# Kernel optimization log

Measured on AMD Instinct MI355X. Metric: run time of the kernel, lower is better.

Reference implementation:

```python
import jax, jax.numpy as jnp
import numpy as np

B, L_IMG, L_TXT = 2, 1024, 512
D_IMG, D_TXT = 2048, 1024
NH, NKV, HD = 16, 8, 128
MLP_IMG, MLP_TXT = 8192, 4096
SOFTCAP = 50.0
EPS = 1e-6

def rms_norm(x, scale):
    var = jnp.mean(jnp.square(x), axis=-1, keepdims=True)
    return x * jax.lax.rsqrt(var + EPS) * (1.0 + scale)

def rope(x, positions):
    # x: [B, L, N, H]; positions: [B, L]
    H = x.shape[-1]
    half = H // 2
    freq = jnp.exp(-jnp.log(10000.0) * (jnp.arange(half, dtype=jnp.float32) * 2.0 / H))
    theta = positions[:, :, None].astype(jnp.float32) * freq          # [B, L, half]
    sin = jnp.sin(theta)[:, :, None, :]
    cos = jnp.cos(theta)[:, :, None, :]
    x1, x2 = jnp.split(x, 2, axis=-1)
    return jnp.concatenate([x1 * cos - x2 * sin, x2 * cos + x1 * sin], axis=-1).astype(x.dtype)

def get_qkv(x_norm, positions, wq, wk, wv):
    b, l, _ = x_norm.shape
    q = (x_norm @ wq).reshape(b, l, NH, HD)
    k = (x_norm @ wk).reshape(b, l, NKV, HD)
    v = (x_norm @ wv).reshape(b, l, NKV, HD)
    q = rope(q, positions)
    k = rope(k, positions)
    q = q * (HD ** -0.5)  # query_pre_attn_norm = 'rsqrt_head_dim'
    return q, k, v

def joint_attention(q, k, v, mask):
    # q: [B,T,NH,HD]; k,v: [B,S,NKV,HD]; mask: [B,1,T,S] bool
    b, t, n, h = q.shape
    g = n // NKV
    qg = q.reshape(b, t, NKV, g, h)
    logits = jnp.einsum('btkgh,bskh->bkgts', qg, k)
    logits = jnp.tanh(logits / SOFTCAP) * SOFTCAP  # attn_logits_softcap
    logits = jnp.where(mask[:, :, None], logits, -1e30)  # [B,1,1,T,S] broadcast
    probs = jax.nn.softmax(logits, axis=-1)
    out = jnp.einsum('bkgts,bskh->btkgh', probs, v)
    return out.reshape(b, t, n, h)

def ffn(x, w_gate, w_up, w_down):
    return (jax.nn.gelu(x @ w_gate) * (x @ w_up)) @ w_down

def _mixture_post(attn_proj, residual, pre_ffw_scale, w_gate, w_up, w_down):
    # post_norms=False, dropout=0: h = mlp(norm(attn_proj + x)) + x
    h = attn_proj + residual
    h = rms_norm(h, pre_ffw_scale)
    h = ffn(h, w_gate, w_up, w_down)
    return h + residual

def _block(x_img, x_txt, attn_mask,
           img_pre_attn_scale, img_wq, img_wk, img_wv, img_wo,
           img_pre_ffw_scale, img_w_gate, img_w_up, img_w_down,
           txt_pre_attn_scale, txt_wq, txt_wk, txt_wv, txt_wo,
           txt_pre_ffw_scale, txt_w_gate, txt_w_up, txt_w_down):
    pos_img = jnp.arange(0, L_IMG, dtype=jnp.int32)[None, :]
    pos_txt = jnp.arange(L_IMG, L_IMG + L_TXT, dtype=jnp.int32)[None, :]
    qi, ki, vi = get_qkv(rms_norm(x_img, img_pre_attn_scale), pos_img, img_wq, img_wk, img_wv)
    qt, kt, vt = get_qkv(rms_norm(x_txt, txt_pre_attn_scale), pos_txt, txt_wq, txt_wk, txt_wv)
    q = jnp.concatenate([qi, qt], axis=1)
    k = jnp.concatenate([ki, kt], axis=1)
    v = jnp.concatenate([vi, vt], axis=1)
    attn = joint_attention(q, k, v, attn_mask)  # [B, T, NH, HD]
    b = attn.shape[0]
    attn_flat = attn.reshape(b, L_IMG + L_TXT, NH * HD)
    proj_img = attn_flat[:, :L_IMG, :] @ img_wo
    proj_txt = attn_flat[:, L_IMG:, :] @ txt_wo
    out_img = _mixture_post(proj_img, x_img, img_pre_ffw_scale, img_w_gate, img_w_up, img_w_down)
    out_txt = _mixture_post(proj_txt, x_txt, txt_pre_ffw_scale, txt_w_gate, txt_w_up, txt_w_down)
    return out_img, out_txt

def setup_inputs() -> dict:
    key = jax.random.key(0)
    ks = jax.random.split(key, 32)
    inner = NH * HD
    def w(k, shape, fan_in):
        return jax.random.normal(k, shape, dtype=jnp.float32) / np.sqrt(fan_in)
    inp = {
        'x_img': jax.random.normal(ks[0], (B, L_IMG, D_IMG), dtype=jnp.float32),
        'x_txt': jax.random.normal(ks[1], (B, L_TXT, D_TXT), dtype=jnp.float32),
        'attn_mask': jnp.ones((B, 1, L_IMG + L_TXT, L_IMG + L_TXT), dtype=bool),
        'img_pre_attn_scale': jnp.zeros((D_IMG,), jnp.float32),
        'img_wq': w(ks[2], (D_IMG, inner), D_IMG),
        'img_wk': w(ks[3], (D_IMG, NKV * HD), D_IMG),
        'img_wv': w(ks[4], (D_IMG, NKV * HD), D_IMG),
        'img_wo': w(ks[5], (inner, D_IMG), inner),
        'img_pre_ffw_scale': jnp.zeros((D_IMG,), jnp.float32),
        'img_w_gate': w(ks[6], (D_IMG, MLP_IMG), D_IMG),
        'img_w_up': w(ks[7], (D_IMG, MLP_IMG), D_IMG),
        'img_w_down': w(ks[8], (MLP_IMG, D_IMG), MLP_IMG),
        'txt_pre_attn_scale': jnp.zeros((D_TXT,), jnp.float32),
        'txt_wq': w(ks[9], (D_TXT, inner), D_TXT),
        'txt_wk': w(ks[10], (D_TXT, NKV * HD), D_TXT),
        'txt_wv': w(ks[11], (D_TXT, NKV * HD), D_TXT),
        'txt_wo': w(ks[12], (inner, D_TXT), inner),
        'txt_pre_ffw_scale': jnp.zeros((D_TXT,), jnp.float32),
        'txt_w_gate': w(ks[13], (D_TXT, MLP_TXT), D_TXT),
        'txt_w_up': w(ks[14], (D_TXT, MLP_TXT), D_TXT),
        'txt_w_down': w(ks[15], (MLP_TXT, D_TXT), MLP_TXT),
    }
    return inp

def reference(x_img, x_txt, attn_mask,
              img_pre_attn_scale, img_wq, img_wk, img_wv, img_wo,
              img_pre_ffw_scale, img_w_gate, img_w_up, img_w_down,
              txt_pre_attn_scale, txt_wq, txt_wk, txt_wv, txt_wo,
              txt_pre_ffw_scale, txt_w_gate, txt_w_up, txt_w_down):
    return _block(x_img, x_txt, attn_mask,
                  img_pre_attn_scale, img_wq, img_wk, img_wv, img_wo,
                  img_pre_ffw_scale, img_w_gate, img_w_up, img_w_down,
                  txt_pre_attn_scale, txt_wq, txt_wk, txt_wv, txt_wo,
                  txt_pre_ffw_scale, txt_w_gate, txt_w_up, txt_w_down)
```

## Files before the change

kernel.cpp:

```cpp
#include <hip/hip_runtime.h>
#include <hip/hip_bf16.h>


typedef __hip_bfloat16 bf16;
typedef __attribute__((ext_vector_type(8))) __bf16 bf16x8;
typedef __attribute__((ext_vector_type(4))) float f32x4;

#define DEV __device__ __forceinline__

static constexpr int TT = 1536;
static constexpr int NHQ = 16, NKVH = 8, HDM = 128;

DEV void async_load16(const void* g, void* l) {
  typedef const __attribute__((address_space(1))) void* gas_t;
  typedef __attribute__((address_space(3))) void* las_t;
  __builtin_amdgcn_global_load_lds((gas_t)g, (las_t)l, 16, 0, 0);
}

DEV f32x4 mfma16(bf16x8 a, bf16x8 b, f32x4 c) {
  return __builtin_amdgcn_mfma_f32_16x16x32_bf16(a, b, c, 0, 0, 0);
}

DEV float bf2f(bf16 x) { return __bfloat162float(x); }
DEV bf16  f2bf(float x) { return __float2bfloat16(x); }

struct TJob { const float* src; bf16* dst; int K; int N; };
struct TJobs { TJob j[14]; int cum[15]; };

__global__ __launch_bounds__(256) void wt_transpose(TJobs P) {
  __shared__ bf16 tile[64][65];
  int bid = blockIdx.x;
  int ji = 0;
  while (ji < 13 && bid >= P.cum[ji + 1]) ji++;
  const TJob jb = P.j[ji];
  int rel = bid - P.cum[ji];
  int ntc = jb.N >> 6;
  int tr = rel / ntc, tc = rel - tr * ntc;
  int r0 = tr << 6, c0 = tc << 6;
  int t = threadIdx.x;
  #pragma unroll
  for (int i = 0; i < 16; i++) {
    int idx = i * 256 + t;
    int r = idx >> 6, c = idx & 63;
    tile[c][r] = f2bf(jb.src[(size_t)(r0 + r) * jb.N + c0 + c]);
  }
  __syncthreads();
  #pragma unroll
  for (int i = 0; i < 16; i++) {
    int idx = i * 256 + t;
    int r = idx >> 6, c = idx & 63;
    jb.dst[(size_t)(c0 + r) * jb.K + r0 + c] = tile[r][c];
  }
}

__global__ __launch_bounds__(256) void transpose_v(const bf16* __restrict__ v_all,
                                                   bf16* __restrict__ vt) {
  int st = blockIdx.x, ht = blockIdx.y, bk = blockIdx.z;
  int b = bk >> 3, kv = bk & 7;
  __shared__ bf16 tile[64][65];
  int t = threadIdx.x;
  int s0 = st * 64, h0 = ht * 64;
  #pragma unroll
  for (int i = 0; i < 16; i++) {
    int idx = i * 256 + t;
    int r = idx >> 6, c = idx & 63;
    tile[c][r] = v_all[((size_t)(b * TT + s0 + r) * NKVH + kv) * HDM + h0 + c];
  }
  __syncthreads();
  #pragma unroll
  for (int i = 0; i < 16; i++) {
    int idx = i * 256 + t;
    int r = idx >> 6, c = idx & 63;
    vt[((size_t)bk * HDM + h0 + r) * TT + s0 + c] = tile[r][c];
  }
}

template <int DV>
__global__ __launch_bounds__(256) void rmsnorm_k(const float* __restrict__ x,
                                                 const float* __restrict__ sc,
                                                 bf16* __restrict__ out) {
  const int D = DV * 1024;
  int row = blockIdx.x, t = threadIdx.x;
  const float4* xr = reinterpret_cast<const float4*>(x + (size_t)row * D);
  float4 v[DV];
  float ss = 0.f;
  #pragma unroll
  for (int i = 0; i < DV; i++) {
    v[i] = xr[t + i * 256];
    ss += v[i].x * v[i].x + v[i].y * v[i].y + v[i].z * v[i].z + v[i].w * v[i].w;
  }
  #pragma unroll
  for (int o = 1; o < 64; o <<= 1) ss += __shfl_xor(ss, o);
  __shared__ float red[4];
  if ((t & 63) == 0) red[t >> 6] = ss;
  __syncthreads();
  float r = rsqrtf((red[0] + red[1] + red[2] + red[3]) * (1.0f / D) + 1e-6f);
  bf16* orow = out + (size_t)row * D;
  #pragma unroll
  for (int i = 0; i < DV; i++) {
    int c = (t + i * 256) * 4;
    orow[c + 0] = f2bf(v[i].x * r * (1.f + sc[c + 0]));
    orow[c + 1] = f2bf(v[i].y * r * (1.f + sc[c + 1]));
    orow[c + 2] = f2bf(v[i].z * r * (1.f + sc[c + 2]));
    orow[c + 3] = f2bf(v[i].w * r * (1.f + sc[c + 3]));
  }
}

template <int DV>
__global__ __launch_bounds__(256) void rmsnorm4_k(
    const float* __restrict__ p0, const float* __restrict__ p1,
    const float* __restrict__ p2, const float* __restrict__ p3,
    const float* __restrict__ x, const float* __restrict__ sc,
    bf16* __restrict__ out) {
  const int D = DV * 1024;
  int row = blockIdx.x, t = threadIdx.x;
  size_t rb = (size_t)row * (D / 4);
  const float4* r0 = reinterpret_cast<const float4*>(p0) + rb;
  const float4* r1 = reinterpret_cast<const float4*>(p1) + rb;
  const float4* r2 = reinterpret_cast<const float4*>(p2) + rb;
  const float4* r3 = reinterpret_cast<const float4*>(p3) + rb;
  const float4* xr = reinterpret_cast<const float4*>(x) + rb;
  float4 v[DV];
  float ss = 0.f;
  #pragma unroll
  for (int i = 0; i < DV; i++) {
    int idx = t + i * 256;
    float4 a = r0[idx], b = r1[idx], c = r2[idx], d = r3[idx], e = xr[idx];
    v[i] = make_float4(a.x + b.x + c.x + d.x + e.x, a.y + b.y + c.y + d.y + e.y,
                       a.z + b.z + c.z + d.z + e.z, a.w + b.w + c.w + d.w + e.w);
    ss += v[i].x * v[i].x + v[i].y * v[i].y + v[i].z * v[i].z + v[i].w * v[i].w;
  }
  #pragma unroll
  for (int o = 1; o < 64; o <<= 1) ss += __shfl_xor(ss, o);
  __shared__ float red[4];
  if ((t & 63) == 0) red[t >> 6] = ss;
  __syncthreads();
  float r = rsqrtf((red[0] + red[1] + red[2] + red[3]) * (1.0f / D) + 1e-6f);
  bf16* orow = out + (size_t)row * D;
  #pragma unroll
  for (int i = 0; i < DV; i++) {
    int c = (t + i * 256) * 4;
    orow[c + 0] = f2bf(v[i].x * r * (1.f + sc[c + 0]));
    orow[c + 1] = f2bf(v[i].y * r * (1.f + sc[c + 1]));
    orow[c + 2] = f2bf(v[i].z * r * (1.f + sc[c + 2]));
    orow[c + 3] = f2bf(v[i].w * r * (1.f + sc[c + 3]));
  }
}

__global__ __launch_bounds__(256) void rope_inplace(bf16* __restrict__ x, int lognh,
                                                    float scale) {
  int gid = blockIdx.x * 256 + threadIdx.x;
  int i = gid & 63;
  int rh = gid >> 6;
  int row = rh >> lognh;
  int pos = row >= TT ? row - TT : row;
  float fr = expf(-9.210340371976184f * ((float)(2 * i) * (1.0f / 128.0f)));
  float th = (float)pos * fr;
  float s, c;
  sincosf(th, &s, &c);
  bf16* p = x + (size_t)rh * HDM;
  float x1 = bf2f(p[i]), x2 = bf2f(p[i + 64]);
  p[i]      = f2bf((x1 * c - x2 * s) * scale);
  p[i + 64] = f2bf((x2 * c + x1 * s) * scale);
}

struct G8Job {
  const bf16* A; const bf16* B; bf16* Cb; float* Cf;
  int K, N, lda, ldb;
  int a_base, a_lsh, a_lskip;
  int c_base, c_lsh, c_lskip, c_stride;
};
struct G8Jobs { G8Job j[8]; int cum[9]; int nj; };

#define G8_BAR_MFMA(MH, NH)                                        \
  __builtin_amdgcn_s_barrier();                                    \
  asm volatile("s_waitcnt lgkmcnt(0)" ::: "memory");               \
  __builtin_amdgcn_sched_barrier(0);                               \
  __builtin_amdgcn_s_setprio(1);                                   \
  _Pragma("unroll")                                                \
  for (int i = 0; i < 4; i++)                                      \
    _Pragma("unroll")                                              \
    for (int nj2 = 0; nj2 < 2; nj2++)                              \
      _Pragma("unroll")                                            \
      for (int kk = 0; kk < 2; kk++)                               \
        acc[(MH)*4 + i][(NH)*2 + nj2] = mfma16(                    \
            afr[i][kk], bfr[(NH)*2 + nj2][kk],                     \
            acc[(MH)*4 + i][(NH)*2 + nj2]);                        \
  __builtin_amdgcn_s_setprio(0);                                   \
  __builtin_amdgcn_s_barrier();                                    \
  asm volatile("" ::: "memory");

__global__ __launch_bounds__(512, 2) void gemm8(G8Jobs P) {
  extern __shared__ __align__(16) bf16 lds8[];
  int bid = blockIdx.x;
  int ji = 0;
  while (ji < P.nj - 1 && bid >= P.cum[ji + 1]) ji++;
  const G8Job jb = P.j[ji];
  int rel = bid - P.cum[ji];
  int tn = jb.N >> 8;
  int bm = rel / tn, bn = rel - bm * tn;
  const int m0 = bm << 8, n0 = bn << 8;
  const int K = jb.K;
  const int nk = K >> 6;
// ... 59 lines not shown
    for (int ni = 0; ni < 2; ni++) {
      int rb = (browb + ni * 16 + lr) * 64;
      bfr[ni][0] = *reinterpret_cast<const bf16x8*>(bufB + rb + s0);
      bfr[ni][1] = *reinterpret_cast<const bf16x8*>(bufB + rb + s1);
    }
    G8_BAR_MFMA(0, 0)

    #pragma unroll
    for (int ni = 2; ni < 4; ni++) {
      int rb = (browb + ni * 16 + lr) * 64;
      bfr[ni][0] = *reinterpret_cast<const bf16x8*>(bufB + rb + s0);
      bfr[ni][1] = *reinterpret_cast<const bf16x8*>(bufB + rb + s1);
    }
    G8_BAR_MFMA(0, 1)

    #pragma unroll
    for (int i = 0; i < 4; i++) {
      int rb = ((i + 4) * 16 + lr) * 64;
      afr[i][0] = *reinterpret_cast<const bf16x8*>(bufA + rb + s0);
      afr[i][1] = *reinterpret_cast<const bf16x8*>(bufA + rb + s1);
    }
    if (st) { stage(t + 2, 2); stage(t + 2, 3); }
    G8_BAR_MFMA(1, 0)

    if (st) {
      stage(t + 2, 0); stage(t + 2, 1);
      asm volatile("s_waitcnt vmcnt(8)" ::: "memory");
    } else if (t == nk - 2) {
      asm volatile("s_waitcnt vmcnt(0)" ::: "memory");
    }
    G8_BAR_MFMA(1, 1)
  }

  if (jb.Cf) {
    #pragma unroll
    for (int mi = 0; mi < 8; mi++)
      #pragma unroll
      for (int jj = 0; jj < 4; jj++) {
        int m = m0 + wr * 128 + mi * 16 + lk * 4 + jj;
        float* drow = jb.Cf + (size_t)m * jb.c_stride + n0 + wc * 64;
        #pragma unroll
        for (int ni = 0; ni < 4; ni++) drow[ni * 16 + lr] = acc[mi][ni][jj];
      }
  } else {
    #pragma unroll
    for (int mi = 0; mi < 8; mi++)
      #pragma unroll
      for (int jj = 0; jj < 4; jj++) {
        int m = m0 + wr * 128 + mi * 16 + lk * 4 + jj;
        int crow = jb.c_base + m + ((m >> jb.c_lsh) * jb.c_lskip);
        bf16* drow = jb.Cb + (size_t)crow * jb.c_stride + n0 + wc * 64;
        #pragma unroll
        for (int ni = 0; ni < 4; ni++) drow[ni * 16 + lr] = f2bf(acc[mi][ni][jj]);
      }
  }
}

__global__ __launch_bounds__(256) void reduce_down(
    float* __restrict__ oi, const float* __restrict__ q1,
    const float* __restrict__ q2, const float* __restrict__ q3,
    const float* __restrict__ xi, int n4i,
    float* __restrict__ ot, const float* __restrict__ r1,
    const float* __restrict__ xt, int n4t) {
  int tot = n4i + n4t;
  for (int idx = blockIdx.x * 256 + threadIdx.x; idx < tot; idx += gridDim.x * 256) {
    if (idx < n4i) {
      float4 d = ((const float4*)oi)[idx];
      float4 a = ((const float4*)q1)[idx];
      float4 b = ((const float4*)q2)[idx];
      float4 c = ((const float4*)q3)[idx];
      float4 e = ((const float4*)xi)[idx];
      ((float4*)oi)[idx] = make_float4(d.x + a.x + b.x + c.x + e.x,
                                       d.y + a.y + b.y + c.y + e.y,
                                       d.z + a.z + b.z + c.z + e.z,
                                       d.w + a.w + b.w + c.w + e.w);
    } else {
      int i = idx - n4i;
      float4 d = ((const float4*)ot)[i];
      float4 a = ((const float4*)r1)[i];
      float4 e = ((const float4*)xt)[i];
      ((float4*)ot)[i] = make_float4(d.x + a.x + e.x, d.y + a.y + e.y,
                                     d.z + a.z + e.z, d.w + a.w + e.w);
    }
  }
}

__global__ __launch_bounds__(256) void gelu_mul(const bf16* __restrict__ gu_i,
                                                bf16* __restrict__ act_i,
                                                const bf16* __restrict__ gu_t,
                                                bf16* __restrict__ act_t) {
  const int IMG_CH = 2048 * 8192 / 8;
  const int TXT_CH = 1024 * 4096 / 8;
  int idx = blockIdx.x * 256 + threadIdx.x;
  int total = IMG_CH + TXT_CH;
  if (idx >= total) return;
  const bf16* base;
  bf16* abase;
  int half, ci;
  if (idx < IMG_CH) { base = gu_i; abase = act_i; half = 8192; ci = idx; }
  else              { base = gu_t; abase = act_t; half = 4096; ci = idx - IMG_CH; }
  int perrow = half / 8;
  int m = ci / perrow, n8 = ci - m * perrow;
  const bf16* gp = base + (size_t)m * (half * 2) + n8 * 8;
  const bf16* up = gp + half;
  bf16x8 g8 = *reinterpret_cast<const bf16x8*>(gp);
  bf16x8 u8 = *reinterpret_cast<const bf16x8*>(up);
  bf16x8 o8;
  #pragma unroll
  for (int i = 0; i < 8; i++) {
    float g = (float)g8[i], u = (float)u8[i];
    float t = tanhf(0.7978845608028654f * (g + 0.044715f * g * g * g));
    o8[i] = (__bf16)(0.5f * g * (1.f + t) * u);
  }
  *reinterpret_cast<bf16x8*>(abase + (size_t)m * half + n8 * 8) = o8;
}

__global__ __launch_bounds__(256) void attn_k(const bf16* __restrict__ q_all,
                                              const bf16* __restrict__ k_all,
                                              const bf16* __restrict__ vt,
                                              bf16* __restrict__ attn_o) {
  const int qt = blockIdx.x;
  const int n = blockIdx.y;
  const int b = blockIdx.z;
  const int kv = n >> 1;
  const int tid = threadIdx.x, w = tid >> 6, l = tid & 63;
  const int lr = l & 15, lk = l >> 4;
  __shared__ __align__(16) bf16 Ksm[64 * 128];
  __shared__ __align__(16) bf16 Vsm[128 * 64];
  __shared__ __align__(16) bf16 Psm[4][16][72];

  bf16x8 qf[4];
  {
    int t = qt * 64 + w * 16 + lr;
    const bf16* qp = q_all + ((size_t)(b * TT + t) * NHQ + n) * HDM;
    #pragma unroll
    for (int kk = 0; kk < 4; kk++)
      qf[kk] = *reinterpret_cast<const bf16x8*>(qp + kk * 32 + lk * 8);
  }
  f32x4 acc_o[8];
  #pragma unroll
  for (int i = 0; i < 8; i++) acc_o[i] = (f32x4){0.f, 0.f, 0.f, 0.f};
  float den[4] = {0.f, 0.f, 0.f, 0.f};

  for (int st = 0; st < TT / 64; st++) {
    __syncthreads();
    #pragma unroll
    for (int i = 0; i < 4; i++) {
// ... 77 lines not shown
  const float* sc_attn_t = (const float*)d_in[12];
  const float* wq_t = (const float*)d_in[13];
  const float* wk_t = (const float*)d_in[14];
  const float* wv_t = (const float*)d_in[15];
  const float* wo_t = (const float*)d_in[16];
  const float* sc_ffw_t = (const float*)d_in[17];
  const float* wg_t = (const float*)d_in[18];
  const float* wu_t = (const float*)d_in[19];
  const float* wd_t = (const float*)d_in[20];
  float* outp = (float*)d_out;
  float* outp_t = outp + (size_t)2 * 1024 * 2048;

  char* ws = (char*)d_ws;
  size_t off = 0;
  auto alloc = [&](size_t n) {
    char* p = ws + off;
    off += (n + 255) & ~(size_t)255;
    return p;
  };
  bf16* WqT_i = (bf16*)alloc((size_t)2048 * 2048 * 2);
  bf16* WkT_i = (bf16*)alloc((size_t)1024 * 2048 * 2);
  bf16* WvT_i = (bf16*)alloc((size_t)1024 * 2048 * 2);
  bf16* WoT_i = (bf16*)alloc((size_t)2048 * 2048 * 2);
  bf16* WguT_i = (bf16*)alloc((size_t)16384 * 2048 * 2);
  bf16* WdT_i = (bf16*)alloc((size_t)2048 * 8192 * 2);
  bf16* WqT_t = (bf16*)alloc((size_t)2048 * 1024 * 2);
  bf16* WkT_t = (bf16*)alloc((size_t)1024 * 1024 * 2);
  bf16* WvT_t = (bf16*)alloc((size_t)1024 * 1024 * 2);
  bf16* WoT_t = (bf16*)alloc((size_t)1024 * 2048 * 2);
  bf16* WguT_t = (bf16*)alloc((size_t)8192 * 1024 * 2);
  bf16* WdT_t = (bf16*)alloc((size_t)1024 * 4096 * 2);
  bf16* xn_i = (bf16*)alloc((size_t)2048 * 2048 * 2);
  bf16* xn_t = (bf16*)alloc((size_t)1024 * 1024 * 2);
  char* S = (char*)alloc((size_t)112 * 1024 * 1024);
  (void)ws_size;

  const size_t MB = 1024 * 1024;
  bf16* q_all = (bf16*)S;
  bf16* k_all = (bf16*)(S + 12 * MB);
  bf16* v_all = (bf16*)(S + 18 * MB);
  bf16* vtr   = (bf16*)(S + 24 * MB);
  bf16* attn_o= (bf16*)(S + 30 * MB);
  float* wp0 = (float*)(S + 42 * MB);
  float* wp1 = (float*)(S + 62 * MB);
  float* wp2 = (float*)(S + 82 * MB);
  float* wp3 = (float*)S;
  const size_t TXT_OFF = 16 * MB / 4;
  bf16* gu_i  = (bf16*)S;
  bf16* gu_t  = (bf16*)(S + 64 * MB);
  bf16* act_i = (bf16*)(S + 80 * MB);
  bf16* act_t = (bf16*)xn_i;
  float* dp1 = (float*)S;
  float* dp2 = (float*)(S + 16 * MB);
  float* dp3 = (float*)(S + 32 * MB);
  float* dpt = (float*)(S + 48 * MB);

  (void)hipFuncSetAttribute(reinterpret_cast<const void*>(gemm8),
                            hipFuncAttributeMaxDynamicSharedMemorySize, 131072);

  TJobs tj;
  auto setj = [&](int idx, const float* s, bf16* d, int K, int N) {
    tj.j[idx].src = s; tj.j[idx].dst = d; tj.j[idx].K = K; tj.j[idx].N = N;
  };
  setj(0, wq_i, WqT_i, 2048, 2048);
  setj(1, wk_i, WkT_i, 2048, 1024);
  setj(2, wv_i, WvT_i, 2048, 1024);
  setj(3, wo_i, WoT_i, 2048, 2048);
  setj(4, wg_i, WguT_i, 2048, 8192);
  setj(5, wu_i, WguT_i + (size_t)8192 * 2048, 2048, 8192);
  setj(6, wd_i, WdT_i, 8192, 2048);
  setj(7, wq_t, WqT_t, 1024, 2048);
  setj(8, wk_t, WkT_t, 1024, 1024);
  setj(9, wv_t, WvT_t, 1024, 1024);
  setj(10, wo_t, WoT_t, 2048, 1024);
  setj(11, wg_t, WguT_t, 1024, 4096);
  setj(12, wu_t, WguT_t + (size_t)4096 * 1024, 1024, 4096);
  setj(13, wd_t, WdT_t, 4096, 1024);
  tj.cum[0] = 0;
  for (int i = 0; i < 14; i++)
    tj.cum[i + 1] = tj.cum[i] + (tj.j[i].K >> 6) * (tj.j[i].N >> 6);
  wt_transpose<<<tj.cum[14], 256, 0, stream>>>(tj);

  rmsnorm_k<2><<<2048, 256, 0, stream>>>(x_img, sc_attn_i, xn_i);
  rmsnorm_k<1><<<1024, 256, 0, stream>>>(x_txt, sc_attn_t, xn_t);

  auto mk8b = [](const bf16* A, const bf16* B, bf16* Cb, int K, int N, int lda,
                 int ldb, int ab, int ash, int ask, int cb2, int csh, int csk,
                 int cstr) {
    G8Job g{};
    g.A = A; g.B = B; g.Cb = Cb; g.Cf = nullptr;
    g.K = K; g.N = N; g.lda = lda; g.ldb = ldb;
    g.a_base = ab; g.a_lsh = ash; g.a_lskip = ask;
    g.c_base = cb2; g.c_lsh = csh; g.c_lskip = csk; g.c_stride = cstr;
    return g;
  };
  auto mk8f = [](const bf16* A, const bf16* B, float* Cf, int K, int N, int lda,
                 int ldb, int ab, int ash, int ask, int cstr) {
    G8Job g{};
    g.A = A; g.B = B; g.Cb = nullptr; g.Cf = Cf;
    g.K = K; g.N = N; g.lda = lda; g.ldb = ldb;
    g.a_base = ab; g.a_lsh = ash; g.a_lskip = ask;
    g.c_base = 0; g.c_lsh = 30; g.c_lskip = 0; g.c_stride = cstr;
    return g;
  };
  auto launch8 = [&](G8Jobs& P, int nj, const int* Mt) {
    P.nj = nj;
    P.cum[0] = 0;
    for (int i = 0; i < nj; i++) P.cum[i + 1] = P.cum[i] + Mt[i] * (P.j[i].N >> 8);
    gemm8<<<P.cum[nj], 512, 131072, stream>>>(P);
  };

  {
    G8Jobs P;
    P.j[0] = mk8b(xn_i, WqT_i, q_all, 2048, 2048, 2048, 2048, 0, 30, 0, 0, 10, 512, 2048);
    P.j[1] = mk8b(xn_i, WkT_i, k_all, 2048, 1024, 2048, 2048, 0, 30, 0, 0, 10, 512, 1024);
    P.j[2] = mk8b(xn_i, WvT_i, v_all, 2048, 1024, 2048, 2048, 0, 30, 0, 0, 10, 512, 1024);
    P.j[3] = mk8b(xn_t, WqT_t, q_all, 1024, 2048, 1024, 1024, 0, 30, 0, 1024, 9, 1024, 2048);
    P.j[4] = mk8b(xn_t, WkT_t, k_all, 1024, 1024, 1024, 1024, 0, 30, 0, 1024, 9, 1024, 1024);
    P.j[5] = mk8b(xn_t, WvT_t, v_all, 1024, 1024, 1024, 1024, 0, 30, 0, 1024, 9, 1024, 1024);
    int Mt[6] = {8, 8, 8, 4, 4, 4};
    launch8(P, 6, Mt);
  }

  rope_inplace<<<12288, 256, 0, stream>>>(q_all, 4, 0.08838834764831845f);
  rope_inplace<<<6144, 256, 0, stream>>>(k_all, 3, 1.0f);

  transpose_v<<<dim3(24, 2, 16), 256, 0, stream>>>(v_all, vtr);

  attn_k<<<dim3(24, 16, 2), 256, 0, stream>>>(q_all, k_all, vtr, attn_o);

  {
    G8Jobs P;
    float* wp[4] = {wp0, wp1, wp2, wp3};
    for (int s = 0; s < 4; s++) {
      P.j[s] = mk8f(attn_o + s * 512, WoT_i + s * 512, wp[s], 512, 2048, 2048,
                    2048, 0, 10, 512, 2048);
      P.j[4 + s] = mk8f(attn_o + s * 512, WoT_t + s * 512, wp[s] + TXT_OFF, 512,
                        1024, 2048, 2048, 1024, 9, 1024, 1024);
    }
    int Mt[8] = {8, 8, 8, 8, 4, 4, 4, 4};
    launch8(P, 8, Mt);
  }

  rmsnorm4_k<2><<<2048, 256, 0, stream>>>(wp0, wp1, wp2, wp3, x_img, sc_ffw_i, xn_i);
  rmsnorm4_k<1><<<1024, 256, 0, stream>>>(wp0 + TXT_OFF, wp1 + TXT_OFF,
                                          wp2 + TXT_OFF, wp3 + TXT_OFF, x_txt,
                                          sc_ffw_t, xn_t);

  {
    G8Jobs P;
    P.j[0] = mk8b(xn_i, WguT_i, gu_i, 2048, 16384, 2048, 2048, 0, 30, 0, 0, 30, 0, 16384);
    int Mt[1] = {8};
    launch8(P, 1, Mt);
  }
  {
    G8Jobs P;
    P.j[0] = mk8b(xn_t, WguT_t, gu_t, 1024, 8192, 1024, 1024, 0, 30, 0, 0, 30, 0, 8192);
    int Mt[1] = {4};
    launch8(P, 1, Mt);
  }
  {
    int total = 2048 * 8192 / 8 + 1024 * 4096 / 8;
    gelu_mul<<<(total + 255) / 256, 256, 0, stream>>>(gu_i, act_i, gu_t, act_t);
  }

  {
    G8Jobs P;
    P.j[0] = mk8f(act_i,            WdT_i,            outp, 2048, 2048, 8192, 8192, 0, 30, 0, 2048);
    P.j[1] = mk8f(act_i + 2048,     WdT_i + 2048,     dp1,  2048, 2048, 8192, 8192, 0, 30, 0, 2048);
    P.j[2] = mk8f(act_i + 4096,     WdT_i + 4096,     dp2,  2048, 2048, 8192, 8192, 0, 30, 0, 2048);
    P.j[3] = mk8f(act_i + 6144,     WdT_i + 6144,     dp3,  2048, 2048, 8192, 8192, 0, 30, 0, 2048);
    P.j[4] = mk8f(act_t,            WdT_t,            outp_t, 2048, 1024, 4096, 4096, 0, 30, 0, 1024);
    P.j[5] = mk8f(act_t + 2048,     WdT_t + 2048,     dpt,  2048, 1024, 4096, 4096, 0, 30, 0, 1024);
    int Mt[6] = {8, 8, 8, 8, 4, 4};
    launch8(P, 6, Mt);
  }
  reduce_down<<<2048, 256, 0, stream>>>(outp, dp1, dp2, dp3, x_img, 2048 * 2048 / 4,
                                        outp_t, dpt, x_txt, 1024 * 1024 / 4);
}
```

Measured before the change: 688.4 us.

## Fuse GELU-gated multiply into gate/up GEMM epilogue and rebalance split-K

Gate and up weight rows are interleaved in 128-column blocks, so each gemm8 tile holds matching gate and up outputs. The epilogue swaps the up half through LDS and writes the GELU(g)*u bf16 activation directly, which removes the standalone gelu_mul kernel and the round trip of the wide gate/up intermediate through global memory. The output projection split-K drops from 4 to 2 partials, so the residual RMSNorm reads fewer buffers. The text down-projection goes from 2 to 4 split-K slices to add parallelism. The fused epilogue adds an LDS exchange and a barrier, and leaves half the waves idle during the writeback.

```diff
diff --git a/kernel.cpp b/kernel.cpp
--- a/kernel.cpp
+++ b/kernel.cpp
@@ -24,7 +24,7 @@
 DEV float bf2f(bf16 x) { return __bfloat162float(x); }
 DEV bf16  f2bf(float x) { return __float2bfloat16(x); }
 
-struct TJob { const float* src; bf16* dst; int K; int N; };
+struct TJob { const float* src; bf16* dst; int K; int N; int r_base, r_lsh, r_skip; };
 struct TJobs { TJob j[14]; int cum[15]; };
 
 __global__ __launch_bounds__(256) void wt_transpose(TJobs P) {
@@ -49,7 +49,9 @@
   for (int i = 0; i < 16; i++) {
     int idx = i * 256 + t;
     int r = idx >> 6, c = idx & 63;
-    jb.dst[(size_t)(c0 + r) * jb.K + r0 + c] = tile[r][c];
+    int n = c0 + r;
+    int phys = jb.r_base + n + ((n >> jb.r_lsh) * jb.r_skip);
+    jb.dst[(size_t)phys * jb.K + r0 + c] = tile[r][c];
   }
 }
 
@@ -107,9 +109,8 @@
 }
 
 template <int DV>
-__global__ __launch_bounds__(256) void rmsnorm4_k(
+__global__ __launch_bounds__(256) void rmsnorm2_k(
     const float* __restrict__ p0, const float* __restrict__ p1,
-    const float* __restrict__ p2, const float* __restrict__ p3,
     const float* __restrict__ x, const float* __restrict__ sc,
     bf16* __restrict__ out) {
   const int D = DV * 1024;
@@ -117,17 +118,15 @@
   size_t rb = (size_t)row * (D / 4);
   const float4* r0 = reinterpret_cast<const float4*>(p0) + rb;
   const float4* r1 = reinterpret_cast<const float4*>(p1) + rb;
-  const float4* r2 = reinterpret_cast<const float4*>(p2) + rb;
-  const float4* r3 = reinterpret_cast<const float4*>(p3) + rb;
   const float4* xr = reinterpret_cast<const float4*>(x) + rb;
   float4 v[DV];
   float ss = 0.f;
   #pragma unroll
   for (int i = 0; i < DV; i++) {
     int idx = t + i * 256;
-    float4 a = r0[idx], b = r1[idx], c = r2[idx], d = r3[idx], e = xr[idx];
-    v[i] = make_float4(a.x + b.x + c.x + d.x + e.x, a.y + b.y + c.y + d.y + e.y,
-                       a.z + b.z + c.z + d.z + e.z, a.w + b.w + c.w + d.w + e.w);
+    float4 a = r0[idx], b = r1[idx], e = xr[idx];
+    v[i] = make_float4(a.x + b.x + e.x, a.y + b.y + e.y,
+                       a.z + b.z + e.z, a.w + b.w + e.w);
     ss += v[i].x * v[i].x + v[i].y * v[i].y + v[i].z * v[i].z + v[i].w * v[i].w;
   }
   #pragma unroll
@@ -169,6 +168,7 @@
   int K, N, lda, ldb;
   int a_base, a_lsh, a_lskip;
   int c_base, c_lsh, c_lskip, c_stride;
+  int fuse;
 };
 struct G8Jobs { G8Job j[8]; int cum[9]; int nj; };
 
@@ -294,7 +294,41 @@
     G8_BAR_MFMA(1, 1)
   }
 
-  if (jb.Cf) {
+  if (jb.fuse) {
+    float* xch = reinterpret_cast<float*>(lds8);
+    if (wc >= 2) {
+      float* slot = xch + (wr * 2 + (wc - 2)) * 8192;
+      #pragma unroll
+      for (int mi = 0; mi < 8; mi++)
+        #pragma unroll
+        for (int jj = 0; jj < 4; jj++) {
+          int row = mi * 16 + lk * 4 + jj;
+          #pragma unroll
+          for (int ni = 0; ni < 4; ni++)
+            slot[row * 64 + ni * 16 + lr] = acc[mi][ni][jj];
+        }
+    }
+    __syncthreads();
+    if (wc < 2) {
+      const float* slot = xch + (wr * 2 + wc) * 8192;
+      int colbase = (n0 >> 1) + wc * 64;
+      #pragma unroll
+      for (int mi = 0; mi < 8; mi++)
+        #pragma unroll
+        for (int jj = 0; jj < 4; jj++) {
+          int m = m0 + wr * 128 + mi * 16 + lk * 4 + jj;
+          int row = mi * 16 + lk * 4 + jj;
+          bf16* drow = jb.Cb + (size_t)m * jb.c_stride + colbase;
+          #pragma unroll
+          for (int ni = 0; ni < 4; ni++) {
+            float g = acc[mi][ni][jj];
+            float u = slot[row * 64 + ni * 16 + lr];
+            float tt = tanhf(0.7978845608028654f * (g + 0.044715f * g * g * g));
+            drow[ni * 16 + lr] = f2bf(0.5f * g * (1.f + tt) * u);
+          }
+        }
+    }
+  } else if (jb.Cf) {
     #pragma unroll
     for (int mi = 0; mi < 8; mi++)
       #pragma unroll
@@ -319,18 +353,19 @@
 }
 
 __global__ __launch_bounds__(256) void reduce_down(
-    float* __restrict__ oi, const float* __restrict__ q1,
-    const float* __restrict__ q2, const float* __restrict__ q3,
+    float* __restrict__ oi, const float* __restrict__ a1,
+    const float* __restrict__ a2, const float* __restrict__ a3,
     const float* __restrict__ xi, int n4i,
-    float* __restrict__ ot, const float* __restrict__ r1,
+    float* __restrict__ ot, const float* __restrict__ b1,
+    const float* __restrict__ b2, const float* __restrict__ b3,
     const float* __restrict__ xt, int n4t) {
   int tot = n4i + n4t;
   for (int idx = blockIdx.x * 256 + threadIdx.x; idx < tot; idx += gridDim.x * 256) {
     if (idx < n4i) {
       float4 d = ((const float4*)oi)[idx];
-      float4 a = ((const float4*)q1)[idx];
-      float4 b = ((const float4*)q2)[idx];
-      float4 c = ((const float4*)q3)[idx];
+      float4 a = ((const float4*)a1)[idx];
+      float4 b = ((const float4*)a2)[idx];
+      float4 c = ((const float4*)a3)[idx];
       float4 e = ((const float4*)xi)[idx];
       ((float4*)oi)[idx] = make_float4(d.x + a.x + b.x + c.x + e.x,
                                        d.y + a.y + b.y + c.y + e.y,
@@ -339,42 +374,16 @@
     } else {
       int i = idx - n4i;
       float4 d = ((const float4*)ot)[i];
-      float4 a = ((const float4*)r1)[i];
+      float4 a = ((const float4*)b1)[i];
+      float4 b = ((const float4*)b2)[i];
+      float4 c = ((const float4*)b3)[i];
       float4 e = ((const float4*)xt)[i];
-      ((float4*)ot)[i] = make_float4(d.x + a.x + e.x, d.y + a.y + e.y,
-                                     d.z + a.z + e.z, d.w + a.w + e.w);
-    }
-  }
-}
-
-__global__ __launch_bounds__(256) void gelu_mul(const bf16* __restrict__ gu_i,
-                                                bf16* __restrict__ act_i,
-                                                const bf16* __restrict__ gu_t,
-                                                bf16* __restrict__ act_t) {
-  const int IMG_CH = 2048 * 8192 / 8;
-  const int TXT_CH = 1024 * 4096 / 8;
-  int idx = blockIdx.x * 256 + threadIdx.x;
-  int total = IMG_CH + TXT_CH;
-  if (idx >= total) return;
-  const bf16* base;
-  bf16* abase;
-  int half, ci;
-  if (idx < IMG_CH) { base = gu_i; abase = act_i; half = 8192; ci = idx; }
-  else              { base = gu_t; abase = act_t; half = 4096; ci = idx - IMG_CH; }
-  int perrow = half / 8;
-  int m = ci / perrow, n8 = ci - m * perrow;
-  const bf16* gp = base + (size_t)m * (half * 2) + n8 * 8;
-  const bf16* up = gp + half;
-  bf16x8 g8 = *reinterpret_cast<const bf16x8*>(gp);
-  bf16x8 u8 = *reinterpret_cast<const bf16x8*>(up);
-  bf16x8 o8;
-  #pragma unroll
-  for (int i = 0; i < 8; i++) {
-    float g = (float)g8[i], u = (float)u8[i];
-    float t = tanhf(0.7978845608028654f * (g + 0.044715f * g * g * g));
-    o8[i] = (__bf16)(0.5f * g * (1.f + t) * u);
-  }
-  *reinterpret_cast<bf16x8*>(abase + (size_t)m * half + n8 * 8) = o8;
+      ((float4*)ot)[i] = make_float4(d.x + a.x + b.x + c.x + e.x,
+                                     d.y + a.y + b.y + c.y + e.y,
+                                     d.z + a.z + b.z + c.z + e.z,
+                                     d.w + a.w + b.w + c.w + e.w);
+    }
+  }
 }
 
 __global__ __launch_bounds__(256) void attn_k(const bf16* __restrict__ q_all,
@@ -529,39 +538,39 @@
   bf16* attn_o= (bf16*)(S + 30 * MB);
   float* wp0 = (float*)(S + 42 * MB);
   float* wp1 = (float*)(S + 62 * MB);
-  float* wp2 = (float*)(S + 82 * MB);
-  float* wp3 = (float*)S;
   const size_t TXT_OFF = 16 * MB / 4;
-  bf16* gu_i  = (bf16*)S;
-  bf16* gu_t  = (bf16*)(S + 64 * MB);
-  bf16* act_i = (bf16*)(S + 80 * MB);
-  bf16* act_t = (bf16*)xn_i;
-  float* dp1 = (float*)S;
-  float* dp2 = (float*)(S + 16 * MB);
-  float* dp3 = (float*)(S + 32 * MB);
-  float* dpt = (float*)(S + 48 * MB);
+  bf16* act_i = (bf16*)S;
+  bf16* act_t = (bf16*)(S + 32 * MB);
+  float* dp1 = (float*)(S + 42 * MB);
+  float* dp2 = (float*)(S + 58 * MB);
+  float* dp3 = (float*)(S + 74 * MB);
+  float* dt1 = (float*)(S + 90 * MB);
+  float* dt2 = (float*)(S + 94 * MB);
+  float* dt3 = (float*)(S + 98 * MB);
 
   (void)hipFuncSetAttribute(reinterpret_cast<const void*>(gemm8),
                             hipFuncAttributeMaxDynamicSharedMemorySize, 131072);
 
   TJobs tj;
-  auto setj = [&](int idx, const float* s, bf16* d, int K, int N) {
+  auto setj = [&](int idx, const float* s, bf16* d, int K, int N, int rb, int rl,
+                  int rs) {
     tj.j[idx].src = s; tj.j[idx].dst = d; tj.j[idx].K = K; tj.j[idx].N = N;
+    tj.j[idx].r_base = rb; tj.j[idx].r_lsh = rl; tj.j[idx].r_skip = rs;
   };
-  setj(0, wq_i, WqT_i, 2048, 2048);
-  setj(1, wk_i, WkT_i, 2048, 1024);
-  setj(2, wv_i, WvT_i, 2048, 1024);
-  setj(3, wo_i, WoT_i, 2048, 2048);
-  setj(4, wg_i, WguT_i, 2048, 8192);
-  setj(5, wu_i, WguT_i + (size_t)8192 * 2048, 2048, 8192);
-  setj(6, wd_i, WdT_i, 8192, 2048);
-  setj(7, wq_t, WqT_t, 1024, 2048);
-  setj(8, wk_t, WkT_t, 1024, 1024);
-  setj(9, wv_t, WvT_t, 1024, 1024);
-  setj(10, wo_t, WoT_t, 2048, 1024);
-  setj(11, wg_t, WguT_t, 1024, 4096);
-  setj(12, wu_t, WguT_t + (size_t)4096 * 1024, 1024, 4096);
-  setj(13, wd_t, WdT_t, 4096, 1024);
+  setj(0, wq_i, WqT_i, 2048, 2048, 0, 30, 0);
+  setj(1, wk_i, WkT_i, 2048, 1024, 0, 30, 0);
+  setj(2, wv_i, WvT_i, 2048, 1024, 0, 30, 0);
+  setj(3, wo_i, WoT_i, 2048, 2048, 0, 30, 0);
+  setj(4, wg_i, WguT_i, 2048, 8192, 0, 7, 128);
+  setj(5, wu_i, WguT_i, 2048, 8192, 128, 7, 128);
+  setj(6, wd_i, WdT_i, 8192, 2048, 0, 30, 0);
+  setj(7, wq_t, WqT_t, 1024, 2048, 0, 30, 0);
+  setj(8, wk_t, WkT_t, 1024, 1024, 0, 30, 0);
+  setj(9, wv_t, WvT_t, 1024, 1024, 0, 30, 0);
+  setj(10, wo_t, WoT_t, 2048, 1024, 0, 30, 0);
+  setj(11, wg_t, WguT_t, 1024, 4096, 0, 7, 128);
+  setj(12, wu_t, WguT_t, 1024, 4096, 128, 7, 128);
+  setj(13, wd_t, WdT_t, 4096, 1024, 0, 30, 0);
   tj.cum[0] = 0;
   for (int i = 0; i < 14; i++)
     tj.cum[i + 1] = tj.cum[i] + (tj.j[i].K >> 6) * (tj.j[i].N >> 6);
@@ -572,12 +581,13 @@
 
   auto mk8b = [](const bf16* A, const bf16* B, bf16* Cb, int K, int N, int lda,
                  int ldb, int ab, int ash, int ask, int cb2, int csh, int csk,
-                 int cstr) {
+                 int cstr, int fuse) {
     G8Job g{};
     g.A = A; g.B = B; g.Cb = Cb; g.Cf = nullptr;
     g.K = K; g.N = N; g.lda = lda; g.ldb = ldb;
     g.a_base = ab; g.a_lsh = ash; g.a_lskip = ask;
     g.c_base = cb2; g.c_lsh = csh; g.c_lskip = csk; g.c_stride = cstr;
+    g.fuse = fuse;
     return g;
   };
   auto mk8f = [](const bf16* A, const bf16* B, float* Cf, int K, int N, int lda,
@@ -587,6 +597,7 @@
     g.K = K; g.N = N; g.lda = lda; g.ldb = ldb;
     g.a_base = ab; g.a_lsh = ash; g.a_lskip = ask;
     g.c_base = 0; g.c_lsh = 30; g.c_lskip = 0; g.c_stride = cstr;
+    g.fuse = 0;
     return g;
   };
   auto launch8 = [&](G8Jobs& P, int nj, const int* Mt) {
@@ -598,12 +609,12 @@
 
   {
     G8Jobs P;
-    P.j[0] = mk8b(xn_i, WqT_i, q_all, 2048, 2048, 2048, 2048, 0, 30, 0, 0, 10, 512, 2048);
-    P.j[1] = mk8b(xn_i, WkT_i, k_all, 2048, 1024, 2048, 2048, 0, 30, 0, 0, 10, 512, 1024);
-    P.j[2] = mk8b(xn_i, WvT_i, v_all, 2048, 1024, 2048, 2048, 0, 30, 0, 0, 10, 512, 1024);
-    P.j[3] = mk8b(xn_t, WqT_t, q_all, 1024, 2048, 1024, 1024, 0, 30, 0, 1024, 9, 1024, 2048);
-    P.j[4] = mk8b(xn_t, WkT_t, k_all, 1024, 1024, 1024, 1024, 0, 30, 0, 1024, 9, 1024, 1024);
-    P.j[5] = mk8b(xn_t, WvT_t, v_all, 1024, 1024, 1024, 1024, 0, 30, 0, 1024, 9, 1024, 1024);
+    P.j[0] = mk8b(xn_i, WqT_i, q_all, 2048, 2048, 2048, 2048, 0, 30, 0, 0, 10, 512, 2048, 0);
+    P.j[1] = mk8b(xn_i, WkT_i, k_all, 2048, 1024, 2048, 2048, 0, 30, 0, 0, 10, 512, 1024, 0);
+    P.j[2] = mk8b(xn_i, WvT_i, v_all, 2048, 1024, 2048, 2048, 0, 30, 0, 0, 10, 512, 1024, 0);
+    P.j[3] = mk8b(xn_t, WqT_t, q_all, 1024, 2048, 1024, 1024, 0, 30, 0, 1024, 9, 1024, 2048, 0);
+    P.j[4] = mk8b(xn_t, WkT_t, k_all, 1024, 1024, 1024, 1024, 0, 30, 0, 1024, 9, 1024, 1024, 0);
+    P.j[5] = mk8b(xn_t, WvT_t, v_all, 1024, 1024, 1024, 1024, 0, 30, 0, 1024, 9, 1024, 1024, 0);
     int Mt[6] = {8, 8, 8, 4, 4, 4};
     launch8(P, 6, Mt);
   }
@@ -617,50 +628,44 @@
 
   {
     G8Jobs P;
-    float* wp[4] = {wp0, wp1, wp2, wp3};
-    for (int s = 0; s < 4; s++) {
-      P.j[s] = mk8f(attn_o + s * 512, WoT_i + s * 512, wp[s], 512, 2048, 2048,
-                    2048, 0, 10, 512, 2048);
-      P.j[4 + s] = mk8f(attn_o + s * 512, WoT_t + s * 512, wp[s] + TXT_OFF, 512,
-                        1024, 2048, 2048, 1024, 9, 1024, 1024);
-    }
+    P.j[0] = mk8f(attn_o,        WoT_i,        wp0, 1024, 2048, 2048, 2048, 0, 10, 512, 2048);
+    P.j[1] = mk8f(attn_o + 1024, WoT_i + 1024, wp1, 1024, 2048, 2048, 2048, 0, 10, 512, 2048);
+    P.j[2] = mk8f(attn_o,        WoT_t,        wp0 + TXT_OFF, 1024, 1024, 2048, 2048, 1024, 9, 1024, 1024);
+    P.j[3] = mk8f(attn_o + 1024, WoT_t + 1024, wp1 + TXT_OFF, 1024, 1024, 2048, 2048, 1024, 9, 1024, 1024);
+    int Mt[4] = {8, 8, 4, 4};
+    launch8(P, 4, Mt);
+  }
+
+  rmsnorm2_k<2><<<2048, 256, 0, stream>>>(wp0, wp1, x_img, sc_ffw_i, xn_i);
+  rmsnorm2_k<1><<<1024, 256, 0, stream>>>(wp0 + TXT_OFF, wp1 + TXT_OFF, x_txt,
+                                          sc_ffw_t, xn_t);
+
+  {
+    G8Jobs P;
+    P.j[0] = mk8b(xn_i, WguT_i, act_i, 2048, 16384, 2048, 2048, 0, 30, 0, 0, 30, 0, 8192, 1);
+    int Mt[1] = {8};
+    launch8(P, 1, Mt);
+  }
+  {
+    G8Jobs P;
+    P.j[0] = mk8b(xn_t, WguT_t, act_t, 1024, 8192, 1024, 1024, 0, 30, 0, 0, 30, 0, 4096, 1);
+    int Mt[1] = {4};
+    launch8(P, 1, Mt);
+  }
+
+  {
+    G8Jobs P;
+    P.j[0] = mk8f(act_i,        WdT_i,        outp, 2048, 2048, 8192, 8192, 0, 30, 0, 2048);
+    P.j[1] = mk8f(act_i + 2048, WdT_i + 2048, dp1,  2048, 2048, 8192, 8192, 0, 30, 0, 2048);
+    P.j[2] = mk8f(act_i + 4096, WdT_i + 4096, dp2,  2048, 2048, 8192, 8192, 0, 30, 0, 2048);
+    P.j[3] = mk8f(act_i + 6144, WdT_i + 6144, dp3,  2048, 2048, 8192, 8192, 0, 30, 0, 2048);
+    P.j[4] = mk8f(act_t,        WdT_t,        outp_t, 1024, 1024, 4096, 4096, 0, 30, 0, 1024);
+    P.j[5] = mk8f(act_t + 1024, WdT_t + 1024, dt1,  1024, 1024, 4096, 4096, 0, 30, 0, 1024);
+    P.j[6] = mk8f(act_t + 2048, WdT_t + 2048, dt2,  1024, 1024, 4096, 4096, 0, 30, 0, 1024);
+    P.j[7] = mk8f(act_t + 3072, WdT_t + 3072, dt3,  1024, 1024, 4096, 4096, 0, 30, 0, 1024);
     int Mt[8] = {8, 8, 8, 8, 4, 4, 4, 4};
     launch8(P, 8, Mt);
   }
-
-  rmsnorm4_k<2><<<2048, 256, 0, stream>>>(wp0, wp1, wp2, wp3, x_img, sc_ffw_i, xn_i);
-  rmsnorm4_k<1><<<1024, 256, 0, stream>>>(wp0 + TXT_OFF, wp1 + TXT_OFF,
-                                          wp2 + TXT_OFF, wp3 + TXT_OFF, x_txt,
-                                          sc_ffw_t, xn_t);
-
-  {
-    G8Jobs P;
-    P.j[0] = mk8b(xn_i, WguT_i, gu_i, 2048, 16384, 2048, 2048, 0, 30, 0, 0, 30, 0, 16384);
-    int Mt[1] = {8};
-    launch8(P, 1, Mt);
-  }
-  {
-    G8Jobs P;
-    P.j[0] = mk8b(xn_t, WguT_t, gu_t, 1024, 8192, 1024, 1024, 0, 30, 0, 0, 30, 0, 8192);
-    int Mt[1] = {4};
-    launch8(P, 1, Mt);
-  }
-  {
-    int total = 2048 * 8192 / 8 + 1024 * 4096 / 8;
-    gelu_mul<<<(total + 255) / 256, 256, 0, stream>>>(gu_i, act_i, gu_t, act_t);
-  }
-
-  {
-    G8Jobs P;
-    P.j[0] = mk8f(act_i,            WdT_i,            outp, 2048, 2048, 8192, 8192, 0, 30, 0, 2048);
-    P.j[1] = mk8f(act_i + 2048,     WdT_i + 2048,     dp1,  2048, 2048, 8192, 8192, 0, 30, 0, 2048);
-    P.j[2] = mk8f(act_i + 4096,     WdT_i + 4096,     dp2,  2048, 2048, 8192, 8192, 0, 30, 0, 2048);
-    P.j[3] = mk8f(act_i + 6144,     WdT_i + 6144,     dp3,  2048, 2048, 8192, 8192, 0, 30, 0, 2048);
-    P.j[4] = mk8f(act_t,            WdT_t,            outp_t, 2048, 1024, 4096, 4096, 0, 30, 0, 1024);
-    P.j[5] = mk8f(act_t + 2048,     WdT_t + 2048,     dpt,  2048, 1024, 4096, 4096, 0, 30, 0, 1024);
-    int Mt[6] = {8, 8, 8, 8, 4, 4};
-    launch8(P, 6, Mt);
-  }
   reduce_down<<<2048, 256, 0, stream>>>(outp, dp1, dp2, dp3, x_img, 2048 * 2048 / 4,
-                                        outp_t, dpt, x_txt, 1024 * 1024 / 4);
-}
+                                        outp_t, dt1, dt2, dt3, x_txt, 1024 * 1024 / 4);
+}
```

Result: no change. 698.1 us (+1.4%).

## Rebalance split-K partitions and fuse img/txt gate-up GEMMs into one launch

Applied to the files above, without the earlier changes.

The output-projection split-K drops from four to two partitions, so the residual RMS norm reads two partial buffers instead of four. The image and text gate/up GEMMs now go out in a single grouped launch rather than two. GELU-mul writes its result in place into the gate half of the gate/up buffer, and the down projection reads it with stride 16384. The text down projection is split four ways instead of two, with its partial sums placed in transposed-weight buffers that are no longer needed. This trades fewer launches and less partial-sum traffic for longer per-tile K loops on the output projection, and it relies on reusing dead weight buffers as scratch.

```diff
diff --git a/kernel.cpp b/kernel.cpp
--- a/kernel.cpp
+++ b/kernel.cpp
@@ -107,9 +107,8 @@
 }
 
 template <int DV>
-__global__ __launch_bounds__(256) void rmsnorm4_k(
+__global__ __launch_bounds__(256) void rmsnorm2_k(
     const float* __restrict__ p0, const float* __restrict__ p1,
-    const float* __restrict__ p2, const float* __restrict__ p3,
     const float* __restrict__ x, const float* __restrict__ sc,
     bf16* __restrict__ out) {
   const int D = DV * 1024;
@@ -117,17 +116,15 @@
   size_t rb = (size_t)row * (D / 4);
   const float4* r0 = reinterpret_cast<const float4*>(p0) + rb;
   const float4* r1 = reinterpret_cast<const float4*>(p1) + rb;
-  const float4* r2 = reinterpret_cast<const float4*>(p2) + rb;
-  const float4* r3 = reinterpret_cast<const float4*>(p3) + rb;
   const float4* xr = reinterpret_cast<const float4*>(x) + rb;
   float4 v[DV];
   float ss = 0.f;
   #pragma unroll
   for (int i = 0; i < DV; i++) {
     int idx = t + i * 256;
-    float4 a = r0[idx], b = r1[idx], c = r2[idx], d = r3[idx], e = xr[idx];
-    v[i] = make_float4(a.x + b.x + c.x + d.x + e.x, a.y + b.y + c.y + d.y + e.y,
-                       a.z + b.z + c.z + d.z + e.z, a.w + b.w + c.w + d.w + e.w);
+    float4 a = r0[idx], b = r1[idx], e = xr[idx];
+    v[i] = make_float4(a.x + b.x + e.x, a.y + b.y + e.y,
+                       a.z + b.z + e.z, a.w + b.w + e.w);
     ss += v[i].x * v[i].x + v[i].y * v[i].y + v[i].z * v[i].z + v[i].w * v[i].w;
   }
   #pragma unroll
@@ -319,18 +316,19 @@
 }
 
 __global__ __launch_bounds__(256) void reduce_down(
-    float* __restrict__ oi, const float* __restrict__ q1,
-    const float* __restrict__ q2, const float* __restrict__ q3,
+    float* __restrict__ oi, const float* __restrict__ a1,
+    const float* __restrict__ a2, const float* __restrict__ a3,
     const float* __restrict__ xi, int n4i,
-    float* __restrict__ ot, const float* __restrict__ r1,
+    float* __restrict__ ot, const float* __restrict__ b1,
+    const float* __restrict__ b2, const float* __restrict__ b3,
     const float* __restrict__ xt, int n4t) {
   int tot = n4i + n4t;
   for (int idx = blockIdx.x * 256 + threadIdx.x; idx < tot; idx += gridDim.x * 256) {
     if (idx < n4i) {
       float4 d = ((const float4*)oi)[idx];
-      float4 a = ((const float4*)q1)[idx];
-      float4 b = ((const float4*)q2)[idx];
-      float4 c = ((const float4*)q3)[idx];
+      float4 a = ((const float4*)a1)[idx];
+      float4 b = ((const float4*)a2)[idx];
+      float4 c = ((const float4*)a3)[idx];
       float4 e = ((const float4*)xi)[idx];
       ((float4*)oi)[idx] = make_float4(d.x + a.x + b.x + c.x + e.x,
                                        d.y + a.y + b.y + c.y + e.y,
@@ -339,32 +337,34 @@
     } else {
       int i = idx - n4i;
       float4 d = ((const float4*)ot)[i];
-      float4 a = ((const float4*)r1)[i];
+      float4 a = ((const float4*)b1)[i];
+      float4 b = ((const float4*)b2)[i];
+      float4 c = ((const float4*)b3)[i];
       float4 e = ((const float4*)xt)[i];
-      ((float4*)ot)[i] = make_float4(d.x + a.x + e.x, d.y + a.y + e.y,
-                                     d.z + a.z + e.z, d.w + a.w + e.w);
-    }
-  }
-}
-
-__global__ __launch_bounds__(256) void gelu_mul(const bf16* __restrict__ gu_i,
-                                                bf16* __restrict__ act_i,
-                                                const bf16* __restrict__ gu_t,
-                                                bf16* __restrict__ act_t) {
+      ((float4*)ot)[i] = make_float4(d.x + a.x + b.x + c.x + e.x,
+                                     d.y + a.y + b.y + c.y + e.y,
+                                     d.z + a.z + b.z + c.z + e.z,
+                                     d.w + a.w + b.w + c.w + e.w);
+    }
+  }
+}
+
+__global__ __launch_bounds__(256) void gelu_mul(bf16* __restrict__ gu_i,
+                                                bf16* __restrict__ gu_t) {
   const int IMG_CH = 2048 * 8192 / 8;
   const int TXT_CH = 1024 * 4096 / 8;
   int idx = blockIdx.x * 256 + threadIdx.x;
   int total = IMG_CH + TXT_CH;
   if (idx >= total) return;
-  const bf16* base;
-  bf16* abase;
+  bf16* base;
   int half, ci;
-  if (idx < IMG_CH) { base = gu_i; abase = act_i; half = 8192; ci = idx; }
-  else              { base = gu_t; abase = act_t; half = 4096; ci = idx - IMG_CH; }
+  if (idx < IMG_CH) { base = gu_i; half = 8192; ci = idx; }
+  else              { base = gu_t; half = 4096; ci = idx - IMG_CH; }
+  int rowlen = half * 2;
   int perrow = half / 8;
   int m = ci / perrow, n8 = ci - m * perrow;
-  const bf16* gp = base + (size_t)m * (half * 2) + n8 * 8;
-  const bf16* up = gp + half;
+  bf16* gp = base + (size_t)m * rowlen + n8 * 8;
+  bf16* up = gp + half;
   bf16x8 g8 = *reinterpret_cast<const bf16x8*>(gp);
   bf16x8 u8 = *reinterpret_cast<const bf16x8*>(up);
   bf16x8 o8;
@@ -374,7 +374,7 @@
     float t = tanhf(0.7978845608028654f * (g + 0.044715f * g * g * g));
     o8[i] = (__bf16)(0.5f * g * (1.f + t) * u);
   }
-  *reinterpret_cast<bf16x8*>(abase + (size_t)m * half + n8 * 8) = o8;
+  *reinterpret_cast<bf16x8*>(gp) = o8;
 }
 
 __global__ __launch_bounds__(256) void attn_k(const bf16* __restrict__ q_all,
@@ -518,7 +518,9 @@
   bf16* WdT_t = (bf16*)alloc((size_t)1024 * 4096 * 2);
   bf16* xn_i = (bf16*)alloc((size_t)2048 * 2048 * 2);
   bf16* xn_t = (bf16*)alloc((size_t)1024 * 1024 * 2);
-  char* S = (char*)alloc((size_t)112 * 1024 * 1024);
+  float* h_i = (float*)alloc((size_t)2048 * 2048 * 4);
+  float* h_t = (float*)alloc((size_t)1024 * 1024 * 4);
+  char* S = (char*)alloc((size_t)84 * 1024 * 1024);
   (void)ws_size;
 
   const size_t MB = 1024 * 1024;
@@ -527,19 +529,16 @@
   bf16* v_all = (bf16*)(S + 18 * MB);
   bf16* vtr   = (bf16*)(S + 24 * MB);
   bf16* attn_o= (bf16*)(S + 30 * MB);
-  float* wp0 = (float*)(S + 42 * MB);
-  float* wp1 = (float*)(S + 62 * MB);
-  float* wp2 = (float*)(S + 82 * MB);
-  float* wp3 = (float*)S;
-  const size_t TXT_OFF = 16 * MB / 4;
+  float* wp1_i = (float*)S;
+  float* wp1_t = (float*)(S + 16 * MB);
   bf16* gu_i  = (bf16*)S;
   bf16* gu_t  = (bf16*)(S + 64 * MB);
-  bf16* act_i = (bf16*)(S + 80 * MB);
-  bf16* act_t = (bf16*)xn_i;
-  float* dp1 = (float*)S;
-  float* dp2 = (float*)(S + 16 * MB);
-  float* dp3 = (float*)(S + 32 * MB);
-  float* dpt = (float*)(S + 48 * MB);
+  float* dp1 = (float*)WguT_i;
+  float* dp2 = (float*)((char*)WguT_i + 16 * MB);
+  float* dp3 = (float*)((char*)WguT_i + 32 * MB);
+  float* dt1 = (float*)WguT_t;
+  float* dt2 = (float*)((char*)WguT_t + 4 * MB);
+  float* dt3 = (float*)((char*)WguT_t + 8 * MB);
 
   (void)hipFuncSetAttribute(reinterpret_cast<const void*>(gemm8),
                             hipFuncAttributeMaxDynamicSharedMemorySize, 131072);
@@ -617,50 +616,42 @@
 
   {
     G8Jobs P;
-    float* wp[4] = {wp0, wp1, wp2, wp3};
-    for (int s = 0; s < 4; s++) {
-      P.j[s] = mk8f(attn_o + s * 512, WoT_i + s * 512, wp[s], 512, 2048, 2048,
-                    2048, 0, 10, 512, 2048);
-      P.j[4 + s] = mk8f(attn_o + s * 512, WoT_t + s * 512, wp[s] + TXT_OFF, 512,
-                        1024, 2048, 2048, 1024, 9, 1024, 1024);
-    }
-    int Mt[8] = {8, 8, 8, 8, 4, 4, 4, 4};
-    launch8(P, 8, Mt);
-  }
-
-  rmsnorm4_k<2><<<2048, 256, 0, stream>>>(wp0, wp1, wp2, wp3, x_img, sc_ffw_i, xn_i);
-  rmsnorm4_k<1><<<1024, 256, 0, stream>>>(wp0 + TXT_OFF, wp1 + TXT_OFF,
-                                          wp2 + TXT_OFF, wp3 + TXT_OFF, x_txt,
-                                          sc_ffw_t, xn_t);
+    P.j[0] = mk8f(attn_o,        WoT_i,        h_i,   1024, 2048, 2048, 2048, 0, 10, 512, 2048);
+    P.j[1] = mk8f(attn_o + 1024, WoT_i + 1024, wp1_i, 1024, 2048, 2048, 2048, 0, 10, 512, 2048);
+    P.j[2] = mk8f(attn_o,        WoT_t,        h_t,   1024, 1024, 2048, 2048, 1024, 9, 1024, 1024);
+    P.j[3] = mk8f(attn_o + 1024, WoT_t + 1024, wp1_t, 1024, 1024, 2048, 2048, 1024, 9, 1024, 1024);
+    int Mt[4] = {8, 8, 4, 4};
+    launch8(P, 4, Mt);
+  }
+
+  rmsnorm2_k<2><<<2048, 256, 0, stream>>>(h_i, wp1_i, x_img, sc_ffw_i, xn_i);
+  rmsnorm2_k<1><<<1024, 256, 0, stream>>>(h_t, wp1_t, x_txt, sc_ffw_t, xn_t);
 
   {
     G8Jobs P;
     P.j[0] = mk8b(xn_i, WguT_i, gu_i, 2048, 16384, 2048, 2048, 0, 30, 0, 0, 30, 0, 16384);
-    int Mt[1] = {8};
-    launch8(P, 1, Mt);
-  }
+    P.j[1] = mk8b(xn_t, WguT_t, gu_t, 1024, 8192, 1024, 1024, 0, 30, 0, 0, 30, 0, 8192);
+    int Mt[2] = {8, 4};
+    launch8(P, 2, Mt);
+  }
+  {
+    int total = 2048 * 8192 / 8 + 1024 * 4096 / 8;
+    gelu_mul<<<(total + 255) / 256, 256, 0, stream>>>(gu_i, gu_t);
+  }
+
   {
     G8Jobs P;
-    P.j[0] = mk8b(xn_t, WguT_t, gu_t, 1024, 8192, 1024, 1024, 0, 30, 0, 0, 30, 0, 8192);
-    int Mt[1] = {4};
-    launch8(P, 1, Mt);
-  }
-  {
-    int total = 2048 * 8192 / 8 + 1024 * 4096 / 8;
-    gelu_mul<<<(total + 255) / 256, 256, 0, stream>>>(gu_i, act_i, gu_t, act_t);
-  }
-
-  {
-    G8Jobs P;
-    P.j[0] = mk8f(act_i,            WdT_i,            outp, 2048, 2048, 8192, 8192, 0, 30, 0, 2048);
-    P.j[1] = mk8f(act_i + 2048,     WdT_i + 2048,     dp1,  2048, 2048, 8192, 8192, 0, 30, 0, 2048);
-    P.j[2] = mk8f(act_i + 4096,     WdT_i + 4096,     dp2,  2048, 2048, 8192, 8192, 0, 30, 0, 2048);
-    P.j[3] = mk8f(act_i + 6144,     WdT_i + 6144,     dp3,  2048, 2048, 8192, 8192, 0, 30, 0, 2048);
-    P.j[4] = mk8f(act_t,            WdT_t,            outp_t, 2048, 1024, 4096, 4096, 0, 30, 0, 1024);
-    P.j[5] = mk8f(act_t + 2048,     WdT_t + 2048,     dpt,  2048, 1024, 4096, 4096, 0, 30, 0, 1024);
-    int Mt[6] = {8, 8, 8, 8, 4, 4};
-    launch8(P, 6, Mt);
+    P.j[0] = mk8f(gu_i,        WdT_i,        outp, 2048, 2048, 16384, 8192, 0, 30, 0, 2048);
+    P.j[1] = mk8f(gu_i + 2048, WdT_i + 2048, dp1,  2048, 2048, 16384, 8192, 0, 30, 0, 2048);
+    P.j[2] = mk8f(gu_i + 4096, WdT_i + 4096, dp2,  2048, 2048, 16384, 8192, 0, 30, 0, 2048);
+    P.j[3] = mk8f(gu_i + 6144, WdT_i + 6144, dp3,  2048, 2048, 16384, 8192, 0, 30, 0, 2048);
+    P.j[4] = mk8f(gu_t,        WdT_t,        outp_t, 1024, 1024, 8192, 4096, 0, 30, 0, 1024);
+    P.j[5] = mk8f(gu_t + 1024, WdT_t + 1024, dt1,  1024, 1024, 8192, 4096, 0, 30, 0, 1024);
+    P.j[6] = mk8f(gu_t + 2048, WdT_t + 2048, dt2,  1024, 1024, 8192, 4096, 0, 30, 0, 1024);
+    P.j[7] = mk8f(gu_t + 3072, WdT_t + 3072, dt3,  1024, 1024, 8192, 4096, 0, 30, 0, 1024);
+    int Mt[8] = {8, 8, 8, 8, 4, 4, 4, 4};
+    launch8(P, 8, Mt);
   }
   reduce_down<<<2048, 256, 0, stream>>>(outp, dp1, dp2, dp3, x_img, 2048 * 2048 / 4,
-                                        outp_t, dpt, x_txt, 1024 * 1024 / 4);
-}
+                                        outp_t, dt1, dt2, dt3, x_txt, 1024 * 1024 / 4);
+}
```

Measured after the change: 646.1 us. 1.07x faster.
